# Optimization experiments

Measured on AMD Instinct MI355X. Metric: run time of the kernel, lower is better.

## Reference

```python
import jax, jax.numpy as jnp
import numpy as np

VOCAB = 32000
DIM = 1024
DFF = 4096
NLLM = 3
B, S = 2, 2048
THRESH = 0.98
EPS = 1e-8


def setup_inputs() -> dict:
    key = jax.random.key(0)
    ks = jax.random.split(key, 5)
    x = jax.random.randint(ks[0], (B, S), 0, VOCAB)
    emb = 0.02 * jax.random.normal(ks[1], (VOCAB, DIM), jnp.float32)
    ln_g = jnp.ones((NLLM, DIM), jnp.float32)
    ln_b = jnp.zeros((NLLM, DIM), jnp.float32)
    W1 = 0.002 * jax.random.normal(ks[2], (NLLM, DIM, DFF), jnp.float32)
    b1 = jnp.zeros((NLLM, DFF), jnp.float32)
    W2 = 0.002 * jax.random.normal(ks[3], (NLLM, DFF, DIM), jnp.float32)
    b2 = jnp.zeros((NLLM, DIM), jnp.float32)
    W_out = (1.0 / np.sqrt(DIM)) * jax.random.normal(ks[4], (VOCAB, DIM), jnp.float32)
    return dict(x=x, emb=emb, ln_g=ln_g, ln_b=ln_b, W1=W1, b1=b1, W2=W2, b2=b2, W_out=W_out)


def _layernorm(h, g, b):
    m = jnp.mean(h, axis=-1, keepdims=True)
    v = jnp.var(h, axis=-1, keepdims=True)
    return (h - m) * jax.lax.rsqrt(v + 1e-5) * g + b


def reference(x, emb, ln_g, ln_b, W1, b1, W2, b2, W_out):
    # Cascaded early-exit ensemble. The torch code physically re-packs surviving
    # tokens; since each LLM block here is per-token (residual MLP), a masked
    # formulation computes identical per-token math and is jit-compatible.
    Bb, Ss = x.shape
    T = Bb * Ss
    h = emb[x.reshape(T)]                      # [T, D] token embeddings
    active = jnp.ones((T,), dtype=bool)
    final = jnp.zeros((T, VOCAB), dtype=h.dtype)
    for i in range(NLLM):                      # fixed, small number of LLMs
        hn = _layernorm(h, ln_g[i], ln_b[i])
        mlp = jax.nn.gelu(hn @ W1[i] + b1[i]) @ W2[i] + b2[i]
        h_out = h + mlp                        # [T, D]
        logits = h_out @ W_out.T               # [T, V] shared output head
        cos = jnp.sum(h * h_out, axis=-1) / (
            jnp.linalg.norm(h, axis=-1) * jnp.linalg.norm(h_out, axis=-1) + EPS)
        is_last = (i == NLLM - 1)
        should_exit = cos >= THRESH
        take = active if is_last else (active & should_exit)
        final = jnp.where(take[:, None], logits, final)   # scatter logits for exiting tokens
        active = active & (~take)
        h = jnp.where(active[:, None], h_out, h)          # continuing tokens carry h_out forward
    return final.reshape(Bb, Ss, VOCAB)
```

## Files before the change

kernel.cpp:

```cpp
#include <hip/hip_runtime.h>
#include <hip/hip_bf16.h>
#include <stdint.h>

constexpr int TK   = 4096;
constexpr int DIMC = 1024;
constexpr int DFFC = 4096;
constexpr int VOC  = 32000;
constexpr int NL   = 3;

typedef __attribute__((ext_vector_type(8))) short bf16x8;
typedef __attribute__((ext_vector_type(8))) _Float16 half8;
typedef __attribute__((ext_vector_type(4))) float f32x4;
using u16 = unsigned short;

__device__ __forceinline__ u16 f2bf(float f) {
  unsigned int u = __float_as_uint(f);
  u += 0x7FFF + ((u >> 16) & 1);
  return (u16)(u >> 16);
}

__device__ __forceinline__ void split16(float v, u16& hi, u16& lo) {
  _Float16 a = (_Float16)v;
  _Float16 b = (_Float16)(v - (float)a);
  hi = __builtin_bit_cast(u16, a);
  lo = __builtin_bit_cast(u16, b);
}

__device__ __forceinline__ float gelu_f(float x) {
  float x3 = x * x * x;
  return 0.5f * x * (1.0f + tanhf(0.7978845608028654f * (x + 0.044715f * x3)));
}

__device__ __forceinline__ void gll16(const void* g, void* l) {
  __builtin_amdgcn_global_load_lds(
      (const __attribute__((address_space(1))) unsigned int*)g,
      (__attribute__((address_space(3))) unsigned int*)l, 16, 0, 0);
}

__global__ __launch_bounds__(256) void k_init(const int* __restrict__ x,
    const float* __restrict__ emb, float* __restrict__ h,
    int* __restrict__ surv, int* __restrict__ cnts) {
  const int t = blockIdx.x, tid = threadIdx.x;
  if (t == 0 && tid < 16) cnts[tid] = (tid == 12) ? TK : 0;
  if (tid == 0) surv[t] = t;
  const int tok = x[t];
  ((float4*)(h + (size_t)t * DIMC))[tid] =
      ((const float4*)(emb + (size_t)tok * DIMC))[tid];
}

__global__ __launch_bounds__(256) void k_ln(const float* __restrict__ h,
    const int* __restrict__ surv, const int* __restrict__ pM,
    const float* __restrict__ g, const float* __restrict__ b,
    u16* __restrict__ hn1, u16* __restrict__ hn2) {
  const int bidx = blockIdx.x;
  if (bidx >= *pM) return;
  const int t = surv[bidx];
  const int tid = threadIdx.x;
  const int lane = tid & 63, wid = tid >> 6;
  __shared__ float sm[4];
  float4 v = ((const float4*)(h + (size_t)t * DIMC))[tid];
  float s = v.x + v.y + v.z + v.w;
#pragma unroll
  for (int o = 32; o; o >>= 1) s += __shfl_down(s, o);
  if (lane == 0) sm[wid] = s;
  __syncthreads();
  const float mean = (sm[0] + sm[1] + sm[2] + sm[3]) * (1.0f / DIMC);
  __syncthreads();
  float4 d;
  d.x = v.x - mean; d.y = v.y - mean; d.z = v.z - mean; d.w = v.w - mean;
  float q = d.x * d.x + d.y * d.y + d.z * d.z + d.w * d.w;
#pragma unroll
  for (int o = 32; o; o >>= 1) q += __shfl_down(q, o);
  if (lane == 0) sm[wid] = q;
  __syncthreads();
  const float var = (sm[0] + sm[1] + sm[2] + sm[3]) * (1.0f / DIMC);
  const float rstd = 1.0f / sqrtf(var + 1e-5f);
  float4 gg = ((const float4*)g)[tid];
  float4 bb = ((const float4*)b)[tid];
  float o4[4];
  o4[0] = (d.x * rstd * gg.x + bb.x) * 16.f;
  o4[1] = (d.y * rstd * gg.y + bb.y) * 16.f;
  o4[2] = (d.z * rstd * gg.z + bb.z) * 16.f;
  o4[3] = (d.w * rstd * gg.w + bb.w) * 16.f;
  ushort4 u1, u2;
  split16(o4[0], u1.x, u2.x); split16(o4[1], u1.y, u2.y);
  split16(o4[2], u1.z, u2.z); split16(o4[3], u1.w, u2.w);
  ((ushort4*)(hn1 + (size_t)bidx * DIMC))[tid] = u1;
  ((ushort4*)(hn2 + (size_t)bidx * DIMC))[tid] = u2;
}

__global__ __launch_bounds__(256) void k_splitw(const float* __restrict__ W,
    int K, int N, u16* __restrict__ O1, u16* __restrict__ O2) {
  __shared__ float t[32][33];
  const int bk = blockIdx.x * 32, bn = blockIdx.y * 32;
  const int lx = threadIdx.x & 31, ly = threadIdx.x >> 5;
#pragma unroll
  for (int i = 0; i < 32; i += 8)
    t[ly + i][lx] = W[(size_t)(bk + ly + i) * N + bn + lx];
  __syncthreads();
#pragma unroll
  for (int i = 0; i < 32; i += 8) {
    float v = t[lx][ly + i] * 256.f;
    u16 h1, h2; split16(v, h1, h2);
    const size_t o = (size_t)(bn + ly + i) * K + bk + lx;
    O1[o] = h1; O2[o] = h2;
  }
}

__global__ __launch_bounds__(256) void k_cvtb(const float* __restrict__ in,
    u16* __restrict__ o, int n4) {
  int i = blockIdx.x * blockDim.x + threadIdx.x;
  const int stride = gridDim.x * blockDim.x;
  for (; i < n4; i += stride) {
    float4 v = ((const float4*)in)[i];
    ushort4 u;
    u.x = f2bf(v.x); u.y = f2bf(v.y); u.z = f2bf(v.z); u.w = f2bf(v.w);
    ((ushort4*)o)[i] = u;
  }
}

template<int EPI, int LDK>
__global__ __launch_bounds__(256, 2) void k_mlp(
    const u16* __restrict__ A1, const u16* __restrict__ A2,
    const u16* __restrict__ B1, const u16* __restrict__ B2,
    const int* __restrict__ pM, int Kpart,
    const float* __restrict__ bias,
    u16* __restrict__ O1, u16* __restrict__ O2,
    float* __restrict__ PO, int N, float oscale)
{
  const int M = *pM;
  const int rb = blockIdx.x;
  if (rb * 128 >= M) return;
  const int n0 = blockIdx.y * 128;
  const int kz = blockIdx.z * Kpart;

  __shared__ u16 S[4][128 * 64];
  const int tid = threadIdx.x;
  const int w = tid >> 6, l = tid & 63;

  const int sr = l >> 3;
  const int sc = ((l & 7) ^ sr) * 8;
  const u16* gp[4];
  {
    const u16* gsrc[4] = {A1, A2, B1, B2};
#pragma unroll
    for (int p = 0; p < 4; ++p) {
      const int row0 = (p < 2) ? rb * 128 : n0;
      gp[p] = gsrc[p] + (size_t)(row0 + w * 32 + sr) * LDK + kz + sc;
    }
  }

  const int wr = w >> 1, wc = w & 1;
  const int lr = l & 15, hi = l >> 4;
  const int sw = lr & 7;
  const int swz0 = (hi ^ sw) * 8;
  const int swz1 = ((4 + hi) ^ sw) * 8;
  const int abase = (wr * 64 + lr) * 64;
  const int bbase = (wc * 64 + lr) * 64;

  f32x4 acc[4][4];
#pragma unroll
  for (int mi = 0; mi < 4; ++mi)
#pragma unroll
    for (int ni = 0; ni < 4; ++ni) acc[mi][ni] = (f32x4){0.f, 0.f, 0.f, 0.f};

  const int NT = Kpart / 64;
  for (int kt = 0; kt < NT; ++kt) {
    __syncthreads();
#pragma unroll
    for (int p = 0; p < 4; ++p)
#pragma unroll
      for (int j = 0; j < 4; ++j)
        gll16(gp[p] + (size_t)j * 8 * LDK + kt * 64,
              (void*)&S[p][(w * 32 + j * 8) * 64]);
    __syncthreads();
#pragma unroll
    for (int ks = 0; ks < 2; ++ks) {
      const int kswz = ks ? swz1 : swz0;
      half8 a1[4], a2[4], b1v[4], b2v[4];
#pragma unroll
      for (int mi = 0; mi < 4; ++mi) {
        a1[mi] = *(const half8*)&S[0][abase + mi * 1024 + kswz];
        a2[mi] = *(const half8*)&S[1][abase + mi * 1024 + kswz];
      }
#pragma unroll
      for (int ni = 0; ni < 4; ++ni) {
        b1v[ni] = *(const half8*)&S[2][bbase + ni * 1024 + kswz];
        b2v[ni] = *(const half8*)&S[3][bbase + ni * 1024 + kswz];
      }
#pragma unroll
      for (int mi = 0; mi < 4; ++mi)
#pragma unroll
        for (int ni = 0; ni < 4; ++ni) {
          acc[mi][ni] = __builtin_amdgcn_mfma_f32_16x16x32_f16(a2[mi], b1v[ni], acc[mi][ni], 0, 0, 0);
          acc[mi][ni] = __builtin_amdgcn_mfma_f32_16x16x32_f16(a1[mi], b2v[ni], acc[mi][ni], 0, 0, 0);
          acc[mi][ni] = __builtin_amdgcn_mfma_f32_16x16x32_f16(a1[mi], b1v[ni], acc[mi][ni], 0, 0, 0);
        }
    }
  }

#pragma unroll
  for (int mi = 0; mi < 4; ++mi)
#pragma unroll
    for (int ni = 0; ni < 4; ++ni) {
      const int n = n0 + wc * 64 + ni * 16 + lr;
#pragma unroll
      for (int r = 0; r < 4; ++r) {
        const int m = rb * 128 + wr * 64 + mi * 16 + hi * 4 + r;
        float v = acc[mi][ni][r] * oscale;
        if constexpr (EPI == 0) {
          v = gelu_f(v + bias[n]) * 64.f;
          u16 h1, h2; split16(v, h1, h2);
          O1[(size_t)m * N + n] = h1;
          O2[(size_t)m * N + n] = h2;
        } else {
          PO[(size_t)(blockIdx.z * TK + m) * N + n] = v;
        }
      }
    }
}

__global__ __launch_bounds__(256) void k_decide(
    float* __restrict__ h, const float* __restrict__ p,
    const float* __restrict__ bias,
    const int* __restrict__ surv_in, int* __restrict__ surv_out,
    const int* __restrict__ pM, int* __restrict__ cnts,
    int* __restrict__ exit_idx, u16* __restrict__ hexit,
    int stage)
{
  const int bidx = blockIdx.x;
  if (bidx >= *pM) return;
  const int t = surv_in[bidx];
  const int tid = threadIdx.x;
  const int lane = tid & 63, wid = tid >> 6;
  __shared__ float sm[12];
  __shared__ int sif[2];
  float4 a  = ((const float4*)(h + (size_t)t * DIMC))[tid];
  float4 p0 = ((const float4*)(p + (size_t)bidx * DIMC))[tid];
  float4 p1 = ((const float4*)(p + (size_t)(TK + bidx) * DIMC))[tid];
  float4 bb = ((const float4*)bias)[tid];
  float4 o;
  o.x = a.x + p0.x + p1.x + bb.x;
  o.y = a.y + p0.y + p1.y + bb.y;
  o.z = a.z + p0.z + p1.z + bb.z;
  o.w = a.w + p0.w + p1.w + bb.w;
  float hh = a.x * a.x + a.y * a.y + a.z * a.z + a.w * a.w;
  float ho = a.x * o.x + a.y * o.y + a.z * o.z + a.w * o.w;
  float oo = o.x * o.x + o.y * o.y + o.z * o.z + o.w * o.w;
#pragma unroll
  for (int off = 32; off; off >>= 1) {
    hh += __shfl_down(hh, off);
    ho += __shfl_down(ho, off);
    oo += __shfl_down(oo, off);
  }
  if (lane == 0) { sm[wid] = hh; sm[4 + wid] = ho; sm[8 + wid] = oo; }
  __syncthreads();
  if (tid == 0) {
    int take;
    if (stage == NL - 1) take = 1;
    else {
      const float HH = sm[0] + sm[1] + sm[2] + sm[3];
      const float HO = sm[4] + sm[5] + sm[6] + sm[7];
      const float OO = sm[8] + sm[9] + sm[10] + sm[11];
      const float cosv = HO / (sqrtf(HH) * sqrtf(OO) + 1e-8f);
      take = (cosv >= 0.98f) ? 1 : 0;
    }
    int pos;
    if (take) {
      pos = atomicAdd(&cnts[stage], 1);
      exit_idx[pos] = t;
    } else {
      pos = atomicAdd(&cnts[4 + stage], 1);
      surv_out[pos] = t;
    }
    sif[0] = take; sif[1] = pos;
  }
  __syncthreads();
  if (sif[0]) {
    u16* dst = hexit + (size_t)sif[1] * DIMC;
    ushort4 u;
    u.x = f2bf(o.x); u.y = f2bf(o.y); u.z = f2bf(o.z); u.w = f2bf(o.w);
    ((ushort4*)dst)[tid] = u;
  } else {
    ((float4*)(h + (size_t)t * DIMC))[tid] = o;
  }
}

__global__ __launch_bounds__(256, 2) void k_logits(
    const u16* __restrict__ Ab,
    const u16* __restrict__ Wb,
    const int* __restrict__ exit_idx,
    const int* __restrict__ pcnt,
    float* __restrict__ out)
{
  const int cnt = *pcnt;
  const int rb = blockIdx.x;
  if (rb * 128 >= cnt) return;
  const int cb = blockIdx.y;

  __shared__ u16 S[2][128 * 64];
  const int tid = threadIdx.x;
  const int w = tid >> 6, l = tid & 63;

  const int sr = l >> 3;
  const int sc = ((l & 7) ^ sr) * 8;
  const u16* gp[2];
  gp[0] = Ab + (size_t)(rb * 128 + w * 32 + sr) * DIMC + sc;
  gp[1] = Wb + (size_t)(cb * 128 + w * 32 + sr) * DIMC + sc;

  const int wr = w >> 1, wc = w & 1;
  const int lr = l & 15, hi = l >> 4;
  const int sw = lr & 7;
  const int swz0 = (hi ^ sw) * 8;
  const int swz1 = ((4 + hi) ^ sw) * 8;
  const int abase = (wr * 64 + lr) * 64;
  const int bbase = (wc * 64 + lr) * 64;

  f32x4 acc[4][4];
#pragma unroll
  for (int mi = 0; mi < 4; ++mi)
#pragma unroll
    for (int ni = 0; ni < 4; ++ni) acc[mi][ni] = (f32x4){0.f, 0.f, 0.f, 0.f};

  const int NT = DIMC / 64;
  for (int kt = 0; kt < NT; ++kt) {
    __syncthreads();
#pragma unroll
    for (int p = 0; p < 2; ++p)
#pragma unroll
      for (int j = 0; j < 4; ++j)
        gll16(gp[p] + (size_t)j * 8 * DIMC + kt * 64,
              (void*)&S[p][(w * 32 + j * 8) * 64]);
    __syncthreads();
#pragma unroll
    for (int ks = 0; ks < 2; ++ks) {
      const int kswz = ks ? swz1 : swz0;
      bf16x8 aF[4], bF[4];
#pragma unroll
      for (int mi = 0; mi < 4; ++mi)
        aF[mi] = *(const bf16x8*)&S[0][abase + mi * 1024 + kswz];
#pragma unroll
      for (int ni = 0; ni < 4; ++ni)
        bF[ni] = *(const bf16x8*)&S[1][bbase + ni * 1024 + kswz];
#pragma unroll
      for (int mi = 0; mi < 4; ++mi)
#pragma unroll
        for (int ni = 0; ni < 4; ++ni)
          acc[mi][ni] = __builtin_amdgcn_mfma_f32_16x16x32_bf16(aF[mi], bF[ni], acc[mi][ni], 0, 0, 0);
    }
  }

  const int mvalid = cnt - rb * 128;
#pragma unroll
  for (int mi = 0; mi < 4; ++mi)
#pragma unroll
    for (int r = 0; r < 4; ++r) {
      const int mrow = wr * 64 + mi * 16 + hi * 4 + r;
      if (mrow < mvalid) {
        const int tok = exit_idx[rb * 128 + mrow];
        float* orow = out + (size_t)tok * VOC + cb * 128 + wc * 64 + lr;
#pragma unroll
        for (int ni = 0; ni < 4; ++ni)
          orow[ni * 16] = acc[mi][ni][r];
      }
    }
}

extern "C" void kernel_launch(void* const* d_in, const int* in_sizes, int n_in,
                              void* d_out, int out_size, void* d_ws, size_t ws_size,
                              hipStream_t stream)
{
  const int*   x    = (const int*)d_in[0];
  const float* emb  = (const float*)d_in[1];
  const float* ln_g = (const float*)d_in[2];
  const float* ln_b = (const float*)d_in[3];
  const float* W1   = (const float*)d_in[4];
  const float* b1   = (const float*)d_in[5];
  const float* W2   = (const float*)d_in[6];
  const float* b2   = (const float*)d_in[7];
  const float* Wout = (const float*)d_in[8];
  float* out = (float*)d_out;

  char* p = (char*)d_ws;
  size_t off = 0;
  auto alloc = [&](size_t bytes) -> void* {
    void* r = p + off;
    off += (bytes + 255) & ~(size_t)255;
    return r;
  };
  float* h    = (float*)alloc((size_t)TK * DIMC * 4);
  float* pbuf = (float*)alloc((size_t)2 * TK * DIMC * 4);
  u16* hn1 = (u16*)pbuf;
  u16* hn2 = hn1 + (size_t)TK * DIMC;
  u16* act1 = (u16*)alloc((size_t)TK * DFFC * 2);
  u16* act2 = (u16*)alloc((size_t)TK * DFFC * 2);
  u16* Woutb = (u16*)alloc((size_t)VOC * DIMC * 2);
  u16* W1t = (u16*)alloc((size_t)2 * DFFC * DIMC * 2);
  u16* W2t = (u16*)alloc((size_t)2 * DIMC * DFFC * 2);
  u16* hexit = (u16*)alloc((size_t)TK * DIMC * 2);
  int* exit_idx = (int*)alloc((size_t)TK * 4);
  int* surv_a   = (int*)alloc((size_t)TK * 4);
  int* surv_b   = (int*)alloc((size_t)TK * 4);
  int* cnts     = (int*)alloc(64 * 4);

  k_init<<<TK, 256, 0, stream>>>(x, emb, h, surv_a, cnts);
  k_cvtb<<<2048, 256, 0, stream>>>(Wout, Woutb, VOC * DIMC / 4);
  int* surv_in  = surv_a;
  int* surv_out = surv_b;
  for (int i = 0; i < NL; ++i) {
    const int* pM = (i == 0) ? (cnts + 12) : (cnts + 4 + (i - 1));
    k_ln<<<TK, 256, 0, stream>>>(h, surv_in, pM, ln_g + i * DIMC, ln_b + i * DIMC, hn1, hn2);
    k_splitw<<<dim3(DIMC / 32, DFFC / 32), 256, 0, stream>>>(
        W1 + (size_t)i * DIMC * DFFC, DIMC, DFFC, W1t, W1t + (size_t)DFFC * DIMC);
    k_mlp<0, DIMC><<<dim3(TK / 128, DFFC / 128, 1), 256, 0, stream>>>(
        hn1, hn2, W1t, W1t + (size_t)DFFC * DIMC, pM, DIMC,
        b1 + (size_t)i * DFFC, act1, act2, nullptr, DFFC, 1.f / 4096.f);
    k_splitw<<<dim3(DFFC / 32, DIMC / 32), 256, 0, stream>>>(
        W2 + (size_t)i * DFFC * DIMC, DFFC, DIMC, W2t, W2t + (size_t)DIMC * DFFC);
    k_mlp<1, DFFC><<<dim3(TK / 128, DIMC / 128, 2), 256, 0, stream>>>(
        act1, act2, W2t, W2t + (size_t)DIMC * DFFC, pM, DFFC / 2,
        nullptr, nullptr, nullptr, pbuf, DIMC, 1.f / 16384.f);
    k_decide<<<TK, 256, 0, stream>>>(h, pbuf, b2 + (size_t)i * DIMC,
        surv_in, surv_out, pM, cnts, exit_idx, hexit, i);
    k_logits<<<dim3(TK / 128, VOC / 128), 256, 0, stream>>>(
        hexit, Woutb, exit_idx, cnts + i, out);
    int* tmp = surv_in; surv_in = surv_out; surv_out = tmp;
  }
}
```

Before: 1.498 ms.

## Double-buffer GEMM LDS loads, swizzle workgroup order, enlarge logits tiles

Rewrites the MLP and logits GEMMs so that global-to-LDS loads for the next K-step (now 32 wide) are issued into a second buffer while the current buffer feeds the MFMAs, leaving one barrier per iteration instead of two. It also raises wave priority around the MFMA block and remaps a flat 1D grid with an XCD-style interleaved swizzle for better L2 locality. The logits kernel moves to 256x256 tiles with 512 threads so each weight tile is reused across more exited tokens. Addressing now uses 32-bit offsets from the workspace base, which adds register pressure and could overflow if the workspace grows large.

```diff
diff --git a/kernel.cpp b/kernel.cpp
--- a/kernel.cpp
+++ b/kernel.cpp
@@ -119,44 +119,51 @@
   }
 }
 
-template<int EPI, int LDK>
+template<int EPI>
 __global__ __launch_bounds__(256, 2) void k_mlp(
-    const u16* __restrict__ A1, const u16* __restrict__ A2,
-    const u16* __restrict__ B1, const u16* __restrict__ B2,
-    const int* __restrict__ pM, int Kpart,
+    const u16* __restrict__ wsb,
+    int offA, int pstrA, int lda,
+    int offB, int pstrB, int ldb,
+    int Kpart, const int* __restrict__ pM,
     const float* __restrict__ bias,
-    u16* __restrict__ O1, u16* __restrict__ O2,
-    float* __restrict__ PO, int N, float oscale)
+    u16* __restrict__ O1, u16* __restrict__ O2, int No,
+    float* __restrict__ PO, float osc,
+    int NRB, int NCB)
 {
+  const int nwg = gridDim.x;
+  const int id = blockIdx.x;
+  const int swz = (id & 7) * (nwg >> 3) + (id >> 3);
+  const int cb = swz % NCB;
+  const int r2 = swz / NCB;
+  const int rb = r2 % NRB;
+  const int z  = r2 / NRB;
   const int M = *pM;
-  const int rb = blockIdx.x;
   if (rb * 128 >= M) return;
-  const int n0 = blockIdx.y * 128;
-  const int kz = blockIdx.z * Kpart;
-
-  __shared__ u16 S[4][128 * 64];
-  const int tid = threadIdx.x;
-  const int w = tid >> 6, l = tid & 63;
-
-  const int sr = l >> 3;
-  const int sc = ((l & 7) ^ sr) * 8;
-  const u16* gp[4];
-  {
-    const u16* gsrc[4] = {A1, A2, B1, B2};
-#pragma unroll
-    for (int p = 0; p < 4; ++p) {
-      const int row0 = (p < 2) ? rb * 128 : n0;
-      gp[p] = gsrc[p] + (size_t)(row0 + w * 32 + sr) * LDK + kz + sc;
+  const int n0 = cb * 128;
+  const int kz = z * Kpart;
+
+  __shared__ u16 S[2][16384];
+  const int tid = threadIdx.x, w = tid >> 6, l = tid & 63;
+  const int lr16 = l & 15, hi = l >> 4, lh8 = hi * 8;
+
+  int goff[8], loff[8];
+#pragma unroll
+  for (int q = 0; q < 8; ++q) {
+    const int bi = w * 8 + q;
+    if (bi < 16) {
+      const int pp = bi >> 3, j = bi & 7;
+      goff[q] = offA + pp * pstrA + (rb * 128 + j * 16 + lr16) * lda + lh8;
+      loff[q] = pp * 4096 + j * 512;
+    } else {
+      const int bb = bi - 16, pp = bb >> 3, j = bb & 7;
+      goff[q] = offB + pp * pstrB + (n0 + j * 16 + lr16) * ldb + lh8;
+      loff[q] = 8192 + pp * 4096 + j * 512;
     }
   }
 
   const int wr = w >> 1, wc = w & 1;
-  const int lr = l & 15, hi = l >> 4;
-  const int sw = lr & 7;
-  const int swz0 = (hi ^ sw) * 8;
-  const int swz1 = ((4 + hi) ^ sw) * 8;
-  const int abase = (wr * 64 + lr) * 64;
-  const int bbase = (wc * 64 + lr) * 64;
+  const int rdA = wr * 4 * 512 + l * 8;
+  const int rdB = 8192 + wc * 4 * 512 + l * 8;
 
   f32x4 acc[4][4];
 #pragma unroll
@@ -164,58 +171,147 @@
 #pragma unroll
     for (int ni = 0; ni < 4; ++ni) acc[mi][ni] = (f32x4){0.f, 0.f, 0.f, 0.f};
 
-  const int NT = Kpart / 64;
+  const int NT = Kpart / 32;
+  auto STAGE = [&](int buf, int kt) {
+#pragma unroll
+    for (int q = 0; q < 8; ++q)
+      gll16(wsb + (size_t)(goff[q] + kz + kt * 32), (void*)&S[buf][loff[q]]);
+  };
+
+  STAGE(0, 0);
+  __syncthreads();
   for (int kt = 0; kt < NT; ++kt) {
+    const int cur = kt & 1;
+    if (kt + 1 < NT) STAGE(cur ^ 1, kt + 1);
+    half8 a1[4], a2[4], b1[4], b2[4];
+#pragma unroll
+    for (int mi = 0; mi < 4; ++mi) {
+      a1[mi] = *(const half8*)&S[cur][rdA + mi * 512];
+      a2[mi] = *(const half8*)&S[cur][rdA + 4096 + mi * 512];
+    }
+#pragma unroll
+    for (int ni = 0; ni < 4; ++ni) {
+      b1[ni] = *(const half8*)&S[cur][rdB + ni * 512];
+      b2[ni] = *(const half8*)&S[cur][rdB + 4096 + ni * 512];
+    }
+    __builtin_amdgcn_s_setprio(1);
+#pragma unroll
+    for (int mi = 0; mi < 4; ++mi)
+#pragma unroll
+      for (int ni = 0; ni < 4; ++ni) {
+        acc[mi][ni] = __builtin_amdgcn_mfma_f32_16x16x32_f16(a2[mi], b1[ni], acc[mi][ni], 0, 0, 0);
+        acc[mi][ni] = __builtin_amdgcn_mfma_f32_16x16x32_f16(a1[mi], b2[ni], acc[mi][ni], 0, 0, 0);
+        acc[mi][ni] = __builtin_amdgcn_mfma_f32_16x16x32_f16(a1[mi], b1[ni], acc[mi][ni], 0, 0, 0);
+      }
+    __builtin_amdgcn_s_setprio(0);
     __syncthreads();
-#pragma unroll
-    for (int p = 0; p < 4; ++p)
-#pragma unroll
-      for (int j = 0; j < 4; ++j)
-        gll16(gp[p] + (size_t)j * 8 * LDK + kt * 64,
-              (void*)&S[p][(w * 32 + j * 8) * 64]);
-    __syncthreads();
-#pragma unroll
-    for (int ks = 0; ks < 2; ++ks) {
-      const int kswz = ks ? swz1 : swz0;
-      half8 a1[4], a2[4], b1v[4], b2v[4];
-#pragma unroll
-      for (int mi = 0; mi < 4; ++mi) {
-        a1[mi] = *(const half8*)&S[0][abase + mi * 1024 + kswz];
-        a2[mi] = *(const half8*)&S[1][abase + mi * 1024 + kswz];
-      }
-#pragma unroll
-      for (int ni = 0; ni < 4; ++ni) {
-        b1v[ni] = *(const half8*)&S[2][bbase + ni * 1024 + kswz];
-        b2v[ni] = *(const half8*)&S[3][bbase + ni * 1024 + kswz];
-      }
-#pragma unroll
-      for (int mi = 0; mi < 4; ++mi)
-#pragma unroll
-        for (int ni = 0; ni < 4; ++ni) {
-          acc[mi][ni] = __builtin_amdgcn_mfma_f32_16x16x32_f16(a2[mi], b1v[ni], acc[mi][ni], 0, 0, 0);
-          acc[mi][ni] = __builtin_amdgcn_mfma_f32_16x16x32_f16(a1[mi], b2v[ni], acc[mi][ni], 0, 0, 0);
-          acc[mi][ni] = __builtin_amdgcn_mfma_f32_16x16x32_f16(a1[mi], b1v[ni], acc[mi][ni], 0, 0, 0);
-        }
-    }
   }
 
 #pragma unroll
   for (int mi = 0; mi < 4; ++mi)
 #pragma unroll
     for (int ni = 0; ni < 4; ++ni) {
-      const int n = n0 + wc * 64 + ni * 16 + lr;
+      const int n = n0 + wc * 64 + ni * 16 + lr16;
 #pragma unroll
       for (int r = 0; r < 4; ++r) {
         const int m = rb * 128 + wr * 64 + mi * 16 + hi * 4 + r;
-        float v = acc[mi][ni][r] * oscale;
+        float v = acc[mi][ni][r] * osc;
         if constexpr (EPI == 0) {
           v = gelu_f(v + bias[n]) * 64.f;
           u16 h1, h2; split16(v, h1, h2);
-          O1[(size_t)m * N + n] = h1;
-          O2[(size_t)m * N + n] = h2;
+          O1[(size_t)m * No + n] = h1;
+          O2[(size_t)m * No + n] = h2;
         } else {
-          PO[(size_t)(blockIdx.z * TK + m) * N + n] = v;
+          PO[(size_t)(z * TK + m) * No + n] = v;
         }
+      }
+    }
+}
+
+__global__ __launch_bounds__(512, 2) void k_logits(
+    const u16* __restrict__ wsb, int offA, int offB,
+    const int* __restrict__ pcnt,
+    const int* __restrict__ exit_idx,
+    float* __restrict__ out)
+{
+  const int nwg = gridDim.x;
+  const int id = blockIdx.x;
+  const int swz = (id & 7) * (nwg >> 3) + (id >> 3);
+  const int cb = swz % 125;
+  const int rb = swz / 125;
+  const int cnt = *pcnt;
+  if (rb * 256 >= cnt) return;
+  const int n0 = cb * 256;
+
+  __shared__ u16 S[2][16384];
+  const int tid = threadIdx.x, w = tid >> 6, l = tid & 63;
+  const int lr16 = l & 15, hi = l >> 4, lh8 = hi * 8;
+
+  int goff[4], loff[4];
+#pragma unroll
+  for (int q = 0; q < 4; ++q) {
+    const int bi = w * 4 + q;
+    if (bi < 16) {
+      goff[q] = offA + (rb * 256 + bi * 16 + lr16) * DIMC + lh8;
+      loff[q] = bi * 512;
+    } else {
+      const int j = bi - 16;
+      goff[q] = offB + (n0 + j * 16 + lr16) * DIMC + lh8;
+      loff[q] = 8192 + j * 512;
+    }
+  }
+
+  const int wr = w >> 2, wc = w & 3;
+  const int rdA = wr * 8 * 512 + l * 8;
+  const int rdB = 8192 + wc * 4 * 512 + l * 8;
+
+  f32x4 acc[8][4];
+#pragma unroll
+  for (int mi = 0; mi < 8; ++mi)
+#pragma unroll
+    for (int ni = 0; ni < 4; ++ni) acc[mi][ni] = (f32x4){0.f, 0.f, 0.f, 0.f};
+
+  auto STAGE = [&](int buf, int kt) {
+#pragma unroll
+    for (int q = 0; q < 4; ++q)
+      gll16(wsb + (size_t)(goff[q] + kt * 32), (void*)&S[buf][loff[q]]);
+  };
+
+  STAGE(0, 0);
+  __syncthreads();
+  const int NT = DIMC / 32;
+  for (int kt = 0; kt < NT; ++kt) {
+    const int cur = kt & 1;
+    if (kt + 1 < NT) STAGE(cur ^ 1, kt + 1);
+    bf16x8 aF[8], bF[4];
+#pragma unroll
+    for (int mi = 0; mi < 8; ++mi)
+      aF[mi] = *(const bf16x8*)&S[cur][rdA + mi * 512];
+#pragma unroll
+    for (int ni = 0; ni < 4; ++ni)
+      bF[ni] = *(const bf16x8*)&S[cur][rdB + ni * 512];
+    __builtin_amdgcn_s_setprio(1);
+#pragma unroll
+    for (int mi = 0; mi < 8; ++mi)
+#pragma unroll
+      for (int ni = 0; ni < 4; ++ni)
+        acc[mi][ni] = __builtin_amdgcn_mfma_f32_16x16x32_bf16(aF[mi], bF[ni], acc[mi][ni], 0, 0, 0);
+    __builtin_amdgcn_s_setprio(0);
+    __syncthreads();
+  }
+
+  const int mvalid = cnt - rb * 256;
+#pragma unroll
+  for (int mi = 0; mi < 8; ++mi)
+#pragma unroll
+    for (int r = 0; r < 4; ++r) {
+      const int mrow = wr * 128 + mi * 16 + hi * 4 + r;
+      if (mrow < mvalid) {
+        const int tok = exit_idx[rb * 256 + mrow];
+        float* orow = out + (size_t)tok * VOC + n0 + wc * 64 + lr16;
+#pragma unroll
+        for (int ni = 0; ni < 4; ++ni)
+          orow[ni * 16] = acc[mi][ni][r];
       }
     }
 }
@@ -286,86 +382,6 @@
   }
 }
 
-__global__ __launch_bounds__(256, 2) void k_logits(
-    const u16* __restrict__ Ab,
-    const u16* __restrict__ Wb,
-    const int* __restrict__ exit_idx,
-    const int* __restrict__ pcnt,
-    float* __restrict__ out)
-{
-  const int cnt = *pcnt;
-  const int rb = blockIdx.x;
-  if (rb * 128 >= cnt) return;
-  const int cb = blockIdx.y;
-
-  __shared__ u16 S[2][128 * 64];
-  const int tid = threadIdx.x;
-  const int w = tid >> 6, l = tid & 63;
-
-  const int sr = l >> 3;
-  const int sc = ((l & 7) ^ sr) * 8;
-  const u16* gp[2];
-  gp[0] = Ab + (size_t)(rb * 128 + w * 32 + sr) * DIMC + sc;
-  gp[1] = Wb + (size_t)(cb * 128 + w * 32 + sr) * DIMC + sc;
-
-  const int wr = w >> 1, wc = w & 1;
-  const int lr = l & 15, hi = l >> 4;
-  const int sw = lr & 7;
-  const int swz0 = (hi ^ sw) * 8;
-  const int swz1 = ((4 + hi) ^ sw) * 8;
-  const int abase = (wr * 64 + lr) * 64;
-  const int bbase = (wc * 64 + lr) * 64;
-
-  f32x4 acc[4][4];
-#pragma unroll
-  for (int mi = 0; mi < 4; ++mi)
-#pragma unroll
-    for (int ni = 0; ni < 4; ++ni) acc[mi][ni] = (f32x4){0.f, 0.f, 0.f, 0.f};
-
-  const int NT = DIMC / 64;
-  for (int kt = 0; kt < NT; ++kt) {
-    __syncthreads();
-#pragma unroll
-    for (int p = 0; p < 2; ++p)
-#pragma unroll
-      for (int j = 0; j < 4; ++j)
-        gll16(gp[p] + (size_t)j * 8 * DIMC + kt * 64,
-              (void*)&S[p][(w * 32 + j * 8) * 64]);
-    __syncthreads();
-#pragma unroll
-    for (int ks = 0; ks < 2; ++ks) {
-      const int kswz = ks ? swz1 : swz0;
-      bf16x8 aF[4], bF[4];
-#pragma unroll
-      for (int mi = 0; mi < 4; ++mi)
-        aF[mi] = *(const bf16x8*)&S[0][abase + mi * 1024 + kswz];
-#pragma unroll
-      for (int ni = 0; ni < 4; ++ni)
-        bF[ni] = *(const bf16x8*)&S[1][bbase + ni * 1024 + kswz];
-#pragma unroll
-      for (int mi = 0; mi < 4; ++mi)
-#pragma unroll
-        for (int ni = 0; ni < 4; ++ni)
-          acc[mi][ni] = __builtin_amdgcn_mfma_f32_16x16x32_bf16(aF[mi], bF[ni], acc[mi][ni], 0, 0, 0);
-    }
-  }
-
-  const int mvalid = cnt - rb * 128;
-#pragma unroll
-  for (int mi = 0; mi < 4; ++mi)
-#pragma unroll
-    for (int r = 0; r < 4; ++r) {
-      const int mrow = wr * 64 + mi * 16 + hi * 4 + r;
-      if (mrow < mvalid) {
-        const int tok = exit_idx[rb * 128 + mrow];
-        float* orow = out + (size_t)tok * VOC + cb * 128 + wc * 64 + lr;
-#pragma unroll
-        for (int ni = 0; ni < 4; ++ni)
-          orow[ni * 16] = acc[mi][ni][r];
-      }
-    }
-}
-
 extern "C" void kernel_launch(void* const* d_in, const int* in_sizes, int n_in,
                               void* d_out, int out_size, void* d_ws, size_t ws_size,
                               hipStream_t stream)
@@ -388,12 +404,13 @@
     off += (bytes + 255) & ~(size_t)255;
     return r;
   };
+  u16* wsb = (u16*)d_ws;
   float* h    = (float*)alloc((size_t)TK * DIMC * 4);
   float* pbuf = (float*)alloc((size_t)2 * TK * DIMC * 4);
   u16* hn1 = (u16*)pbuf;
   u16* hn2 = hn1 + (size_t)TK * DIMC;
-  u16* act1 = (u16*)alloc((size_t)TK * DFFC * 2);
-  u16* act2 = (u16*)alloc((size_t)TK * DFFC * 2);
+  u16* act1 = (u16*)alloc((size_t)2 * TK * DFFC * 2);
+  u16* act2 = act1 + (size_t)TK * DFFC;
   u16* Woutb = (u16*)alloc((size_t)VOC * DIMC * 2);
   u16* W1t = (u16*)alloc((size_t)2 * DFFC * DIMC * 2);
   u16* W2t = (u16*)alloc((size_t)2 * DIMC * DFFC * 2);
@@ -402,6 +419,13 @@
   int* surv_a   = (int*)alloc((size_t)TK * 4);
   int* surv_b   = (int*)alloc((size_t)TK * 4);
   int* cnts     = (int*)alloc(64 * 4);
+
+  const int offHn  = (int)(hn1  - wsb);
+  const int offAct = (int)(act1 - wsb);
+  const int offWob = (int)(Woutb- wsb);
+  const int offW1t = (int)(W1t  - wsb);
+  const int offW2t = (int)(W2t  - wsb);
+  const int offHex = (int)(hexit- wsb);
 
   k_init<<<TK, 256, 0, stream>>>(x, emb, h, surv_a, cnts);
   k_cvtb<<<2048, 256, 0, stream>>>(Wout, Woutb, VOC * DIMC / 4);
@@ -412,18 +436,19 @@
     k_ln<<<TK, 256, 0, stream>>>(h, surv_in, pM, ln_g + i * DIMC, ln_b + i * DIMC, hn1, hn2);
     k_splitw<<<dim3(DIMC / 32, DFFC / 32), 256, 0, stream>>>(
         W1 + (size_t)i * DIMC * DFFC, DIMC, DFFC, W1t, W1t + (size_t)DFFC * DIMC);
-    k_mlp<0, DIMC><<<dim3(TK / 128, DFFC / 128, 1), 256, 0, stream>>>(
-        hn1, hn2, W1t, W1t + (size_t)DFFC * DIMC, pM, DIMC,
-        b1 + (size_t)i * DFFC, act1, act2, nullptr, DFFC, 1.f / 4096.f);
+    k_mlp<0><<<1024, 256, 0, stream>>>(
+        wsb, offHn, TK * DIMC, DIMC, offW1t, DFFC * DIMC, DIMC,
+        DIMC, pM, b1 + (size_t)i * DFFC, act1, act2, DFFC,
+        nullptr, 1.f / 4096.f, 32, 32);
     k_splitw<<<dim3(DFFC / 32, DIMC / 32), 256, 0, stream>>>(
         W2 + (size_t)i * DFFC * DIMC, DFFC, DIMC, W2t, W2t + (size_t)DIMC * DFFC);
-    k_mlp<1, DFFC><<<dim3(TK / 128, DIMC / 128, 2), 256, 0, stream>>>(
-        act1, act2, W2t, W2t + (size_t)DIMC * DFFC, pM, DFFC / 2,
-        nullptr, nullptr, nullptr, pbuf, DIMC, 1.f / 16384.f);
+    k_mlp<1><<<512, 256, 0, stream>>>(
+        wsb, offAct, TK * DFFC, DFFC, offW2t, DIMC * DFFC, DFFC,
+        DFFC / 2, pM, nullptr, nullptr, nullptr, DIMC,
+        pbuf, 1.f / 16384.f, 32, 8);
     k_decide<<<TK, 256, 0, stream>>>(h, pbuf, b2 + (size_t)i * DIMC,
         surv_in, surv_out, pM, cnts, exit_idx, hexit, i);
-    k_logits<<<dim3(TK / 128, VOC / 128), 256, 0, stream>>>(
-        hexit, Woutb, exit_idx, cnts + i, out);
+    k_logits<<<2000, 512, 0, stream>>>(wsb, offHex, offWob, cnts + i, exit_idx, out);
     int* tmp = surv_in; surv_in = surv_out; surv_out = tmp;
   }
 }
```

Result: slower. 2.150 ms (+43.6%).
